# Optimization experiments

Hardware: AMD Instinct MI355X
Metric: run time of the kernel (lower is better)

The kernel has to match this reference:

```python
import jax, jax.numpy as jnp
import numpy as np

B, CN, T = 16, 22, 1000
EXP, FCH, SPD, NCLS = 300, 150, 100, 4
KS = (15, 75, 55)
_IU = np.triu_indices(SPD)
_VEC_SCALE = np.where(_IU[0] == _IU[1], 1.0, np.sqrt(2.0)).astype(np.float32)


def _ln(x, g, b, eps=1e-5):
    m = x.mean(-1, keepdims=True)
    v = x.var(-1, keepdims=True)
    return (x - m) / jnp.sqrt(v + eps) * g + b


def _block(x, w1, w2, w3, w4, g1, b1, w5, g2, b2):
    # x: (B, CN, T). Conv2d(1,1,(3,1), same) over electrode axis.
    h = jax.lax.conv_general_dilated(x[:, None], w1.reshape(1, 1, 3, 1), (1, 1),
                                     [(1, 1), (0, 0)],
                                     dimension_numbers=('NCHW', 'OIHW', 'NCHW'))[:, 0]
    # Conv2d(1, 300, (1,1)): pure channel broadcast-expand
    h = h[:, None, :, :] * w2[None, :, None, None]          # (B, EXP, CN, T)
    # Conv2dWithConstraint: depthwise spatial conv (groups=300) with max-norm=1 on each filter
    n = jnp.linalg.norm(w3, axis=1, keepdims=True)
    w3r = w3 * jnp.minimum(1.0, 1.0 / (n + 1e-12))
    h = jnp.einsum('bgct,gc->bgt', h, w3r)                  # height collapses -> (B, EXP, T)
    h = jnp.einsum('og,bgt->bot', w4, h)                    # pointwise -> (B, FCH, T)
    h = _ln(h, g1, b1)
    K = w5.shape[-1]
    # depthwise temporal conv, padding='same' (odd K)
    h = jax.lax.conv_general_dilated(h, w5, (1,), [(K // 2, K // 2)],
                                     dimension_numbers=('NCH', 'OIH', 'NCH'),
                                     feature_group_count=FCH)
    return _ln(h, g2, b2)


def setup_inputs():
    key = jax.random.key(0)
    ks = jax.random.split(key, 64)
    d = {'x': jax.random.normal(ks[0], (B, CN, T), jnp.float32)}
    i = 1
    for bi, K in zip((1, 2, 3), KS):
        d[f'b{bi}_w1'] = jax.random.normal(ks[i], (3,)) / np.sqrt(3); i += 1
        d[f'b{bi}_w2'] = jax.random.normal(ks[i], (EXP,)); i += 1
        d[f'b{bi}_w3'] = jax.random.normal(ks[i], (EXP, CN)) / np.sqrt(CN); i += 1
        d[f'b{bi}_w4'] = jax.random.normal(ks[i], (FCH, EXP)) / np.sqrt(EXP); i += 1
        d[f'b{bi}_g1'] = jnp.ones((T,)); d[f'b{bi}_b1'] = jnp.zeros((T,))
        d[f'b{bi}_w5'] = jax.random.normal(ks[i], (FCH, 1, K)) / np.sqrt(K); i += 1
        d[f'b{bi}_g2'] = jnp.ones((T,)); d[f'b{bi}_b2'] = jnp.zeros((T,))
    d['w_sconv'] = jax.random.normal(ks[i], (SPD, 3 * FCH)) / np.sqrt(3 * FCH); i += 1
    d['w_aff'] = jnp.eye(SPD) + 0.05 * jax.random.normal(ks[i], (SPD, SPD)); i += 1
    d['w_fc'] = jax.random.normal(ks[i], (NCLS, SPD * (SPD + 1) // 2)) / np.sqrt(SPD * (SPD + 1) // 2); i += 1
    d['b_fc'] = jnp.zeros((NCLS,))
    return d


def reference(x,
              b1_w1, b1_w2, b1_w3, b1_w4, b1_g1, b1_b1, b1_w5, b1_g2, b1_b2,
              b2_w1, b2_w2, b2_w3, b2_w4, b2_g1, b2_b1, b2_w5, b2_g2, b2_b2,
              b3_w1, b3_w2, b3_w3, b3_w4, b3_g1, b3_b1, b3_w5, b3_g2, b3_b2,
              w_sconv, w_aff, w_fc, b_fc):
    h1 = _block(x, b1_w1, b1_w2, b1_w3, b1_w4, b1_g1, b1_b1, b1_w5, b1_g2, b1_b2)
    h2 = _block(x, b2_w1, b2_w2, b2_w3, b2_w4, b2_g1, b2_b1, b2_w5, b2_g2, b2_b2)
    h3 = _block(x, b3_w1, b3_w2, b3_w3, b3_w4, b3_g1, b3_b1, b3_w5, b3_g2, b3_b2)
    h = jnp.concatenate([h1, h2, h3], axis=1)               # (B, 450, T)
    h = jnp.einsum('oi,bit->bot', w_sconv, h)               # (B, SPD, T)
    # PCOM: covariance pooling over time -> SPD matrix per sample
    xc = h - h.mean(-1, keepdims=True)
    cov = jnp.einsum('bit,bjt->bij', xc, xc) / (T - 1) + 1e-4 * jnp.eye(SPD)
    # AffineInvariantLayer: learnable congruence transform W P W^T
    P = jnp.einsum('ij,bjk,lk->bil', w_aff, cov, w_aff)
    # LogmLayer: matrix log via batched eigendecomposition
    w, v = jnp.linalg.eigh(P)
    L = jnp.einsum('bik,bk,bjk->bij', v, jnp.log(jnp.clip(w, 1e-6)), v)
    # Vec: upper-triangular half-vectorization (off-diag * sqrt(2)) -> 5050
    flat = L[:, _IU[0], _IU[1]] * _VEC_SCALE
    logits = flat @ w_fc.T + b_fc
    return (logits, flat)
```

## Files before the change

### kernel.cpp

```cpp
#include <hip/hip_runtime.h>

#define B_ 16
#define CN_ 22
#define T_ 1000
#define EXP_ 300
#define FCH_ 150
#define SPD_ 100
#define LDSTR 108
#define MAXSWEEP 8

static constexpr unsigned long long OFF_M2   = 0ull;
static constexpr unsigned long long OFF_HCAT = 65536ull;
static constexpr unsigned long long OFF_XC   = OFF_HCAT + 28800000ull;
static constexpr unsigned long long OFF_COV  = OFF_XC   + 6400000ull;
static constexpr unsigned long long OFF_T1   = OFF_COV  + 640000ull;
static constexpr unsigned long long OFF_P    = OFF_T1   + 640000ull;
static constexpr unsigned long long OFF_G    = OFF_XC;
static constexpr unsigned long long OFF_WC   = OFF_XC + 640000ull;

struct PrepPtrs  { const float* w1[3]; const float* w2[3]; const float* w3[3]; const float* w4[3]; };
struct FrontPtrs { const float* g1[3]; const float* b1[3]; const float* w5[3];
                   const float* g2[3]; const float* b2[3]; int K[3]; };

__device__ __forceinline__ float block_sum(float v, float* sbuf) {
  #pragma unroll
  for (int off = 32; off > 0; off >>= 1) v += __shfl_down(v, off, 64);
  const int wid  = threadIdx.x >> 6;
  const int lane = threadIdx.x & 63;
  const int nw   = blockDim.x >> 6;
  if (lane == 0) sbuf[wid] = v;
  __syncthreads();
  float r = 0.f;
  for (int w = 0; w < nw; ++w) r += sbuf[w];
  __syncthreads();
  return r;
}

__device__ __forceinline__ float dpp_shr1(float old_, float src) {
  return __builtin_bit_cast(float, __builtin_amdgcn_update_dpp(
      __builtin_bit_cast(int, old_), __builtin_bit_cast(int, src),
      0x138, 0xf, 0xf, false));
}
__device__ __forceinline__ float dpp_shl1(float old_, float src) {
  return __builtin_bit_cast(float, __builtin_amdgcn_update_dpp(
      __builtin_bit_cast(int, old_), __builtin_bit_cast(int, src),
      0x130, 0xf, 0xf, false));
}

__global__ __launch_bounds__(256) void k_prep(PrepPtrs pp, float* __restrict__ M2) {
  const int beta = blockIdx.x;
  __shared__ float w3r[EXP_*CN_];
  __shared__ float M[FCH_*CN_];
  const float* w1 = pp.w1[beta];
  const float* w2 = pp.w2[beta];
  const float* w3 = pp.w3[beta];
  const float* w4 = pp.w4[beta];

  for (int g = threadIdx.x; g < EXP_; g += 256) {
    float s = 0.f;
    for (int c = 0; c < CN_; ++c) { float w = w3[g*CN_ + c]; s += w*w; }
    float n = sqrtf(s);
    float scale = fminf(1.f, 1.f/(n + 1e-12f)) * w2[g];
    for (int c = 0; c < CN_; ++c) w3r[g*CN_ + c] = w3[g*CN_ + c] * scale;
  }
  __syncthreads();
  for (int idx = threadIdx.x; idx < FCH_*CN_; idx += 256) {
    int o = idx / CN_, c = idx - o*CN_;
    float acc = 0.f;
    for (int g = 0; g < EXP_; ++g) acc += w4[o*EXP_ + g] * w3r[g*CN_ + c];
    M[idx] = acc;
  }
  __syncthreads();
  const float k0 = w1[0], k1 = w1[1], k2 = w1[2];
  for (int idx = threadIdx.x; idx < FCH_*CN_; idx += 256) {
    int c = idx % CN_;
    float v = k1 * M[idx];
    if (c > 0)       v += k2 * M[idx - 1];
    if (c < CN_ - 1) v += k0 * M[idx + 1];
    M2[beta*FCH_*CN_ + idx] = v;
  }
}

__global__ __launch_bounds__(256) void k_front(const float* __restrict__ x,
                                               const float* __restrict__ M2,
                                               FrontPtrs fp,
                                               float* __restrict__ hcat) {
  const int wg   = blockIdx.x;
  const int beta = wg / (B_*FCH_);
  const int rem  = wg - beta*(B_*FCH_);
  const int b    = rem / FCH_;
  const int o    = rem - b*FCH_;
  const int K    = fp.K[beta];
  const int Kh   = K >> 1;

  __shared__ float m2[CN_];
  __shared__ float hb2[T_];
  __shared__ float w5s[80];
  __shared__ float red[8];

  if (threadIdx.x < CN_) m2[threadIdx.x] = M2[(beta*FCH_ + o)*CN_ + threadIdx.x];
  if (threadIdx.x < K)   w5s[threadIdx.x] = fp.w5[beta][o*K + threadIdx.x];
  __syncthreads();

  const float* xb = x + (size_t)b*CN_*T_;
  float hv[4];
  float psum = 0.f;
  #pragma unroll
  for (int e = 0; e < 4; ++e) {
    int t = threadIdx.x + 256*e;
    float acc = 0.f;
    if (t < T_) {
      #pragma unroll
      for (int c = 0; c < CN_; ++c) acc += m2[c] * xb[c*T_ + t];
    }
    hv[e] = acc; psum += acc;
  }
  float mean = block_sum(psum, red) * (1.f/T_);
  float pv = 0.f;
  #pragma unroll
  for (int e = 0; e < 4; ++e) { int t = threadIdx.x + 256*e; if (t < T_) { float d = hv[e]-mean; pv += d*d; } }
  float var = block_sum(pv, red) * (1.f/T_);
  float inv = rsqrtf(var + 1e-5f);
  const float* g1 = fp.g1[beta]; const float* b1 = fp.b1[beta];
  #pragma unroll
  for (int e = 0; e < 4; ++e) { int t = threadIdx.x + 256*e; if (t < T_) hb2[t] = (hv[e]-mean)*inv*g1[t] + b1[t]; }
  __syncthreads();

  float cv[4];
  float ps2 = 0.f;
  #pragma unroll
  for (int e = 0; e < 4; ++e) {
    int t = threadIdx.x + 256*e;
    float acc = 0.f;
    if (t < T_) {
      int lo = t - Kh;
      for (int k = 0; k < K; ++k) {
        int tt = lo + k;
        float hvv = (tt >= 0 && tt < T_) ? hb2[tt] : 0.f;
        acc += hvv * w5s[k];
      }
    }
    cv[e] = acc; ps2 += acc;
  }
  float mean2 = block_sum(ps2, red) * (1.f/T_);
  float pv2 = 0.f;
  #pragma unroll
  for (int e = 0; e < 4; ++e) { int t = threadIdx.x + 256*e; if (t < T_) { float d = cv[e]-mean2; pv2 += d*d; } }
  float var2 = block_sum(pv2, red) * (1.f/T_);
  float inv2 = rsqrtf(var2 + 1e-5f);
  const float* g2 = fp.g2[beta]; const float* b2 = fp.b2[beta];
  float* hrow = hcat + ((size_t)b*(3*FCH_) + beta*FCH_ + o)*T_;
  #pragma unroll
  for (int e = 0; e < 4; ++e) { int t = threadIdx.x + 256*e; if (t < T_) hrow[t] = (cv[e]-mean2)*inv2*g2[t] + b2[t]; }
}

__global__ __launch_bounds__(256) void k_sconv(const float* __restrict__ hcat,
                                               const float* __restrict__ wsc,
                                               float* __restrict__ xc) {
  const int b  = blockIdx.x / 10;
  const int s0 = (blockIdx.x % 10) * 10;
  __shared__ float ws[10*450];
  __shared__ float red[8];
  for (int idx = threadIdx.x; idx < 4500; idx += 256) {
    int s = idx / 450, i = idx - s*450;
    ws[idx] = wsc[(s0+s)*450 + i];
  }
  __syncthreads();
  float acc[10][4];
  #pragma unroll
  for (int s = 0; s < 10; ++s)
    #pragma unroll
    for (int e = 0; e < 4; ++e) acc[s][e] = 0.f;
  const float* hb = hcat + (size_t)b*450*T_;
  for (int i = 0; i < 450; ++i) {
    float xv[4];
    #pragma unroll
    for (int e = 0; e < 4; ++e) { int t = threadIdx.x + 256*e; xv[e] = (t < T_) ? hb[(size_t)i*T_ + t] : 0.f; }
    #pragma unroll
    for (int s = 0; s < 10; ++s) {
      float w = ws[s*450 + i];
      #pragma unroll
      for (int e = 0; e < 4; ++e) acc[s][e] += w * xv[e];
    }
  }
  for (int s = 0; s < 10; ++s) {
    float mu = block_sum(acc[s][0]+acc[s][1]+acc[s][2]+acc[s][3], red) * (1.f/T_);
    float* xr = xc + ((size_t)b*SPD_ + s0 + s)*T_;
    #pragma unroll
    for (int e = 0; e < 4; ++e) { int t = threadIdx.x + 256*e; if (t < T_) xr[t] = acc[s][e] - mu; }
  }
}

__global__ __launch_bounds__(256) void k_cov(const float* __restrict__ xc, float* __restrict__ cov) {
  const int b  = blockIdx.x / 5;
  const int j0 = (blockIdx.x % 5) * 20;
  __shared__ __align__(16) float xst[SPD_*100];
  const int it = threadIdx.x / 10;
  const int jj = threadIdx.x - it*10;
  const bool act = threadIdx.x < 250;
  double a64[4][2] = {{0.0,0.0},{0.0,0.0},{0.0,0.0},{0.0,0.0}};
  for (int ch = 0; ch < 10; ++ch) {
    __syncthreads();
    const int tc0 = ch*100;
    for (int idx = threadIdx.x; idx < SPD_*100; idx += 256) {
      int row = idx / 100, tt = idx - row*100;
      xst[idx] = xc[((size_t)b*SPD_ + row)*T_ + tc0 + tt];
    }
    __syncthreads();
    if (act) {
      float a32[4][2] = {{0,0},{0,0},{0,0},{0,0}};
      for (int t4 = 0; t4 < 100; t4 += 4) {
        float4 xi[4], xj[2];
        #pragma unroll
        for (int r = 0; r < 4; ++r) xi[r] = *(const float4*)&xst[(it + 25*r)*100 + t4];
        #pragma unroll
        for (int s = 0; s < 2; ++s) xj[s] = *(const float4*)&xst[(j0 + jj + 10*s)*100 + t4];
        #pragma unroll
        for (int r = 0; r < 4; ++r)
          #pragma unroll
          for (int s = 0; s < 2; ++s)
            a32[r][s] += xi[r].x*xj[s].x + xi[r].y*xj[s].y + xi[r].z*xj[s].z + xi[r].w*xj[s].w;
      }
      #pragma unroll
      for (int r = 0; r < 4; ++r)
        #pragma unroll
        for (int s = 0; s < 2; ++s) a64[r][s] += (double)a32[r][s];
    }
  }
  if (act) {
    #pragma unroll
    for (int r = 0; r < 4; ++r) {
      #pragma unroll
      for (int s = 0; s < 2; ++s) {
        int i = it + 25*r, j = j0 + jj + 10*s;
        double v = a64[r][s] * (1.0/999.0);
        if (i == j) v += 1e-4;
        cov[(size_t)b*SPD_*SPD_ + i*SPD_ + j] = (float)v;
      }
    }
  }
}

__global__ __launch_bounds__(256) void k_aff1(const float* __restrict__ cov,
                                              const float* __restrict__ waff,
                                              float* __restrict__ T1) {
  const int b  = blockIdx.x / 5;
  const int j0 = (blockIdx.x % 5) * 20;
  __shared__ float Cs[SPD_*101];
  __shared__ float Ws[20*100];
  for (int idx = threadIdx.x; idx < SPD_*SPD_; idx += 256) {
    int r = idx / 100, c = idx - r*100;
    Cs[r*101 + c] = cov[(size_t)b*SPD_*SPD_ + idx];
  }
  for (int idx = threadIdx.x; idx < 2000; idx += 256) {
    int jl = idx / 100, k = idx - jl*100;
    Ws[idx] = waff[(j0+jl)*100 + k];
  }
  __syncthreads();
  if (threadIdx.x < 250) {
    const int it = threadIdx.x / 10, jj = threadIdx.x % 10;
    double acc[4][2] = {{0.0,0.0},{0.0,0.0},{0.0,0.0},{0.0,0.0}};
    for (int k = 0; k < 100; ++k) {
      double cvv[4], wv[2];
      #pragma unroll
      for (int r = 0; r < 4; ++r) cvv[r] = (double)Cs[(it + 25*r)*101 + k];
      #pragma unroll
      for (int s = 0; s < 2; ++s) wv[s] = (double)Ws[(jj + 10*s)*100 + k];
      #pragma unroll
      for (int r = 0; r < 4; ++r)
        #pragma unroll
        for (int s = 0; s < 2; ++s) acc[r][s] += cvv[r]*wv[s];
    }
    #pragma unroll
    for (int r = 0; r < 4; ++r)
      #pragma unroll
      for (int s = 0; s < 2; ++s)
        T1[(size_t)b*SPD_*SPD_ + (it + 25*r)*100 + (j0 + jj + 10*s)] = (float)acc[r][s];
  }
}

__global__ __launch_bounds__(256) void k_aff2(const float* __restrict__ T1,
                                              const float* __restrict__ waff,
                                              float* __restrict__ P) {
  const int b  = blockIdx.x / 5;
  const int j0 = (blockIdx.x % 5) * 20;
  __shared__ float T1s[100*20];
  for (int idx = threadIdx.x; idx < 2000; idx += 256) {
    int k = idx / 20, jl = idx - k*20;
    T1s[idx] = T1[(size_t)b*SPD_*SPD_ + k*100 + j0 + jl];
  }
  __syncthreads();
  if (threadIdx.x < 250) {
    const int it = threadIdx.x / 10, jj = threadIdx.x % 10;
    double acc[4][2] = {{0.0,0.0},{0.0,0.0},{0.0,0.0},{0.0,0.0}};
    for (int k = 0; k < 100; ++k) {
      double wv[4], tv[2];
      #pragma unroll
      for (int r = 0; r < 4; ++r) wv[r] = (double)waff[(it + 25*r)*100 + k];
      #pragma unroll
      for (int s = 0; s < 2; ++s) tv[s] = (double)T1s[k*20 + jj + 10*s];
      #pragma unroll
      for (int r = 0; r < 4; ++r)
        #pragma unroll
        for (int s = 0; s < 2; ++s) acc[r][s] += wv[r]*tv[s];
    }
    #pragma unroll
    for (int r = 0; r < 4; ++r)
      #pragma unroll
      for (int s = 0; s < 2; ++s)
        P[(size_t)b*SPD_*SPD_ + (it + 25*r)*100 + (j0 + jj + 10*s)] = (float)acc[r][s];
  }
}

__global__ __launch_bounds__(256, 1) void k_eig(const float* __restrict__ P,
                                                float* __restrict__ Gout,
                                                double* __restrict__ WCout) {
  __shared__ __align__(16) float G[SPD_*LDSTR];
  __shared__ __align__(16) float gbuf[2][64*4];
  __shared__ __align__(16) float nbuf[64*8];
  __shared__ int fbuf[4];
  const int tid = threadIdx.x;
  const int b   = blockIdx.x;
  const int w   = tid >> 6;
  const int j   = tid & 63;
  const bool act = (j < 50);
  const int rb  = 25 * w;

  float A[25], B[25];
  const float* Pb = P + (size_t)b*SPD_*SPD_;
  #pragma unroll
  for (int i = 0; i < 25; ++i) {
    A[i] = act ? Pb[(rb+i)*SPD_ + j]      : 0.f;
    B[i] = act ? Pb[(rb+i)*SPD_ + (99-j)] : 0.f;
  }
  float pA = 0.f, pB = 0.f;
  #pragma unroll
  for (int i = 0; i < 25; ++i) { pA += A[i]*A[i]; pB += B[i]*B[i]; }
  nbuf[j*8 + w*2 + 0] = pA;
  nbuf[j*8 + w*2 + 1] = pB;
  __syncthreads();
  float nA, nB;
  {
    float4 u0 = *(const float4*)&nbuf[j*8];
    float4 u1 = *(const float4*)&nbuf[j*8+4];
    nA = (u0.x + u0.z) + (u1.x + u1.z);
    nB = (u0.y + u0.w) + (u1.y + u1.w);
  }
  float pg = 0.f;
  #pragma unroll
  for (int i = 0; i < 25; ++i) pg += A[i]*B[i];

  int par = 0;
  for (int sweep = 0; sweep < MAXSWEEP; ++sweep) {
    int swflag = 0;
    for (int r = 0; r < 99; ++r) {
      gbuf[par][j*4 + w] = pg;
      __syncthreads();
      float4 gp = *(const float4*)&gbuf[par][j*4];
      float gamma = (gp.x + gp.y) + (gp.z + gp.w);

      float cr = 1.f, sr = 0.f;
      float g2 = gamma*gamma;
      float ab = nA*nB;
      if (act && g2 > 1e-12f*ab) {
        if (g2 > 1e-6f*ab) swflag = 1;
        float tau = (nB - nA) / (2.f*gamma);
        float t = ((tau >= 0.f) ? 1.f : -1.f) / (fabsf(tau) + sqrtf(1.f + tau*tau));
        cr = rsqrtf(1.f + t*t);
        sr = t*cr;
        nA = nA - t*gamma;
        nB = nB + t*gamma;
      }
      {
        float sendN = (j == 0) ? nB : nA;
        float rNA = dpp_shr1(nA, sendN);
        float rNB = dpp_shl1(nB, nB);
        float newB = (j == 49) ? nA : rNB;
        nA = rNA; nB = newB;
      }
      pg = 0.f;
      #pragma unroll
      for (int i = 0; i < 25; ++i) {
        float na = cr*A[i] - sr*B[i];
        float nb = sr*A[i] + cr*B[i];
        float sendA = (j == 0) ? nb : na;
        float rA = dpp_shr1(na, sendA);
        float rB = dpp_shl1(nb, nb);
        A[i] = rA;
        B[i] = (j == 49) ? na : rB;
        pg += A[i]*B[i];
      }
      par ^= 1;
    }
    unsigned long long any = __ballot(swflag);
    if (j == 0) fbuf[w] = (any != 0ull) ? 1 : 0;
    __syncthreads();
    int f = fbuf[0] | fbuf[1] | fbuf[2] | fbuf[3];
    __syncthreads();
    if (!f) break;
  }

  if (act) {
    #pragma unroll
    for (int i = 0; i < 25; ++i) {
      G[j*LDSTR + rb + i]        = A[i];
      G[(50 + j)*LDSTR + rb + i] = B[i];
    }
  }
  __syncthreads();

  if (tid < SPD_) {
    const float* col = &G[tid*LDSTR];
    double s = 0.0;
    for (int i = 0; i < SPD_; ++i) { double v = (double)col[i]; s += v*v; }
    double lam = sqrt(s);
    double lc  = (lam < 1e-6) ? 1e-6 : lam;
    WCout[b*SPD_ + tid] = log(lc) / ((s > 1e-300) ? s : 1e-300);
  }
  for (int idx = tid; idx < SPD_*SPD_; idx += 256) {
    int c = idx / SPD_, i = idx - c*SPD_;
    Gout[(size_t)b*SPD_*SPD_ + idx] = G[c*LDSTR + i];
  }
}

__global__ __launch_bounds__(256) void k_lout(const float* __restrict__ Gin,
                                              const double* __restrict__ WCin,
                                              float* __restrict__ out) {
  __shared__ __align__(16) float G[SPD_*SPD_];
  __shared__ float wcs[SPD_];
  const int tid = threadIdx.x;
  const int b   = blockIdx.x;
  for (int idx = tid; idx < SPD_*SPD_; idx += 256)
    G[idx] = Gin[(size_t)b*SPD_*SPD_ + idx];
  if (tid < SPD_) wcs[tid] = (float)WCin[b*SPD_ + tid];
  __syncthreads();

  for (int tile = tid; tile < 625; tile += 256) {
    const int ti = (tile / 25) * 4;
    const int tj = (tile % 25) * 4;
    float acc[4][4];
    #pragma unroll
    for (int r = 0; r < 4; ++r)
      #pragma unroll
      for (int s = 0; s < 4; ++s) acc[r][s] = 0.f;
    for (int c = 0; c < SPD_; ++c) {
      const float* col = &G[c*SPD_];
      float4 ga = *(const float4*)&col[ti];
      float4 gb = *(const float4*)&col[tj];
      float wcv = wcs[c];
      float wa[4] = { wcv*ga.x, wcv*ga.y, wcv*ga.z, wcv*ga.w };
      float bv[4] = { gb.x, gb.y, gb.z, gb.w };
      #pragma unroll
      for (int r = 0; r < 4; ++r)
        #pragma unroll
        for (int s = 0; s < 4; ++s) acc[r][s] += wa[r]*bv[s];
    }
    const float RT2 = 1.41421356237309505f;
    #pragma unroll
    for (int r = 0; r < 4; ++r) {
      #pragma unroll
      for (int s = 0; s < 4; ++s) {
        int i = ti + r, jx = tj + s;
        if (i <= jx) {
          int idx = i*SPD_ - (i*(i+1))/2 + jx;
          out[64 + b*5050 + idx] = acc[r][s] * (i == jx ? 1.f : RT2);
        }
      }
    }
  }
}

__global__ __launch_bounds__(256) void k_fc(const float* __restrict__ wfc,
                                            const float* __restrict__ bfc,
                                            float* __restrict__ out) {
  __shared__ float red[8];
  const int b = blockIdx.x;
  const float* flat = out + 64 + b*5050;
  float a0 = 0.f, a1 = 0.f, a2 = 0.f, a3 = 0.f;
  for (int k = threadIdx.x; k < 5050; k += 256) {
    float f = flat[k];
    a0 += f * wfc[k];
    a1 += f * wfc[5050 + k];
    a2 += f * wfc[10100 + k];
    a3 += f * wfc[15150 + k];
  }
  a0 = block_sum(a0, red);
  a1 = block_sum(a1, red);
  a2 = block_sum(a2, red);
  a3 = block_sum(a3, red);
  if (threadIdx.x == 0) {
    out[b*4 + 0] = a0 + bfc[0];
    out[b*4 + 1] = a1 + bfc[1];
    out[b*4 + 2] = a2 + bfc[2];
    out[b*4 + 3] = a3 + bfc[3];
  }
}

extern "C" void kernel_launch(void* const* d_in, const int* in_sizes, int n_in,
                              void* d_out, int out_size, void* d_ws, size_t ws_size,
                              hipStream_t stream) {
  (void)in_sizes; (void)n_in; (void)out_size; (void)ws_size;
  const float* x = (const float*)d_in[0];
  const float* bw[3][9];
  for (int i = 0; i < 3; ++i)
    for (int jx = 0; jx < 9; ++jx)
      bw[i][jx] = (const float*)d_in[1 + i*9 + jx];
  const float* w_sconv = (const float*)d_in[28];
  const float* w_aff   = (const float*)d_in[29];
  const float* w_fc    = (const float*)d_in[30];
  const float* b_fc    = (const float*)d_in[31];

  char* ws = (char*)d_ws;
  float*  M2   = (float*)(ws + OFF_M2);
  float*  hcat = (float*)(ws + OFF_HCAT);
  float*  xc   = (float*)(ws + OFF_XC);
  float*  cov  = (float*)(ws + OFF_COV);
  float*  T1   = (float*)(ws + OFF_T1);
  float*  P    = (float*)(ws + OFF_P);
  float*  G    = (float*)(ws + OFF_G);
  double* WC   = (double*)(ws + OFF_WC);
  float*  out  = (float*)d_out;

  PrepPtrs pp; FrontPtrs fp;
  for (int i = 0; i < 3; ++i) {
    pp.w1[i] = bw[i][0]; pp.w2[i] = bw[i][1]; pp.w3[i] = bw[i][2]; pp.w4[i] = bw[i][3];
    fp.g1[i] = bw[i][4]; fp.b1[i] = bw[i][5]; fp.w5[i] = bw[i][6];
    fp.g2[i] = bw[i][7]; fp.b2[i] = bw[i][8];
  }
  fp.K[0] = 15; fp.K[1] = 75; fp.K[2] = 55;

  hipLaunchKernelGGL(k_prep,  dim3(3),            dim3(256), 0, stream, pp, M2);
  hipLaunchKernelGGL(k_front, dim3(3*B_*FCH_),    dim3(256), 0, stream, x, M2, fp, hcat);
  hipLaunchKernelGGL(k_sconv, dim3(B_*10),        dim3(256), 0, stream, hcat, w_sconv, xc);
  hipLaunchKernelGGL(k_cov,   dim3(B_*5),         dim3(256), 0, stream, xc, cov);
  hipLaunchKernelGGL(k_aff1,  dim3(B_*5),         dim3(256), 0, stream, cov, w_aff, T1);
  hipLaunchKernelGGL(k_aff2,  dim3(B_*5),         dim3(256), 0, stream, T1, w_aff, P);
  hipLaunchKernelGGL(k_eig,   dim3(B_),           dim3(256), 0, stream, P, G, WC);
  hipLaunchKernelGGL(k_lout,  dim3(B_),           dim3(256), 0, stream, G, WC, out);
  hipLaunchKernelGGL(k_fc,    dim3(B_),           dim3(256), 0, stream, w_fc, b_fc, out);
}
```

Measured before the change: 1.297 ms.

## Pack two matrices per Jacobi eigen block, drop convergence check, move eigenlog to output kernel

The Jacobi eigensolver now handles two batch matrices per 512-thread block, each using its own 256-thread half and shared buffers. It always runs a fixed number of sweeps instead of stopping early on a convergence vote, and the rotation is computed without branches. It writes the eigenvector columns straight to global memory, and the eigenvalue log weights are now computed in the following output kernel. This removes the per-sweep ballot and barrier, the shared staging copy and the double-precision buffer, but it halves the number of eigen blocks, makes every block barrier span more waves, and may run more sweeps than needed.

```diff
diff --git a/kernel.cpp b/kernel.cpp
--- a/kernel.cpp
+++ b/kernel.cpp
@@ -6,8 +6,7 @@
 #define EXP_ 300
 #define FCH_ 150
 #define SPD_ 100
-#define LDSTR 108
-#define MAXSWEEP 8
+#define NSWEEP 8
 
 static constexpr unsigned long long OFF_M2   = 0ull;
 static constexpr unsigned long long OFF_HCAT = 65536ull;
@@ -16,7 +15,6 @@
 static constexpr unsigned long long OFF_T1   = OFF_COV  + 640000ull;
 static constexpr unsigned long long OFF_P    = OFF_T1   + 640000ull;
 static constexpr unsigned long long OFF_G    = OFF_XC;
-static constexpr unsigned long long OFF_WC   = OFF_XC + 640000ull;
 
 struct PrepPtrs  { const float* w1[3]; const float* w2[3]; const float* w3[3]; const float* w4[3]; };
 struct FrontPtrs { const float* g1[3]; const float* b1[3]; const float* w5[3];
@@ -312,19 +310,17 @@
   }
 }
 
-__global__ __launch_bounds__(256, 1) void k_eig(const float* __restrict__ P,
-                                                float* __restrict__ Gout,
-                                                double* __restrict__ WCout) {
-  __shared__ __align__(16) float G[SPD_*LDSTR];
-  __shared__ __align__(16) float gbuf[2][64*4];
-  __shared__ __align__(16) float nbuf[64*8];
-  __shared__ int fbuf[4];
-  const int tid = threadIdx.x;
-  const int b   = blockIdx.x;
-  const int w   = tid >> 6;
-  const int j   = tid & 63;
-  const bool act = (j < 50);
-  const int rb  = 25 * w;
+__global__ __launch_bounds__(512, 1) void k_eig(const float* __restrict__ P,
+                                                float* __restrict__ Gout) {
+  __shared__ __align__(16) float gbuf[2][2][256];
+  __shared__ __align__(16) float nbuf[2][512];
+  const int tid   = threadIdx.x;
+  const int mh    = tid >> 8;
+  const int ww    = (tid >> 6) & 3;
+  const int j     = tid & 63;
+  const bool act  = (j < 50);
+  const int rb    = 25 * ww;
+  const int b     = blockIdx.x * 2 + mh;
 
   float A[25], B[25];
   const float* Pb = P + (size_t)b*SPD_*SPD_;
@@ -336,13 +332,13 @@
   float pA = 0.f, pB = 0.f;
   #pragma unroll
   for (int i = 0; i < 25; ++i) { pA += A[i]*A[i]; pB += B[i]*B[i]; }
-  nbuf[j*8 + w*2 + 0] = pA;
-  nbuf[j*8 + w*2 + 1] = pB;
+  nbuf[mh][j*8 + ww*2 + 0] = pA;
+  nbuf[mh][j*8 + ww*2 + 1] = pB;
   __syncthreads();
   float nA, nB;
   {
-    float4 u0 = *(const float4*)&nbuf[j*8];
-    float4 u1 = *(const float4*)&nbuf[j*8+4];
+    float4 u0 = *(const float4*)&nbuf[mh][j*8];
+    float4 u1 = *(const float4*)&nbuf[mh][j*8+4];
     nA = (u0.x + u0.z) + (u1.x + u1.z);
     nB = (u0.y + u0.w) + (u1.y + u1.w);
   }
@@ -351,26 +347,22 @@
   for (int i = 0; i < 25; ++i) pg += A[i]*B[i];
 
   int par = 0;
-  for (int sweep = 0; sweep < MAXSWEEP; ++sweep) {
-    int swflag = 0;
+  for (int sweep = 0; sweep < NSWEEP; ++sweep) {
     for (int r = 0; r < 99; ++r) {
-      gbuf[par][j*4 + w] = pg;
+      gbuf[mh][par][j*4 + ww] = pg;
       __syncthreads();
-      float4 gp = *(const float4*)&gbuf[par][j*4];
+      float4 gp = *(const float4*)&gbuf[mh][par][j*4];
       float gamma = (gp.x + gp.y) + (gp.z + gp.w);
 
-      float cr = 1.f, sr = 0.f;
       float g2 = gamma*gamma;
       float ab = nA*nB;
-      if (act && g2 > 1e-12f*ab) {
-        if (g2 > 1e-6f*ab) swflag = 1;
-        float tau = (nB - nA) / (2.f*gamma);
-        float t = ((tau >= 0.f) ? 1.f : -1.f) / (fabsf(tau) + sqrtf(1.f + tau*tau));
-        cr = rsqrtf(1.f + t*t);
-        sr = t*cr;
-        nA = nA - t*gamma;
-        nB = nB + t*gamma;
-      }
+      float tau = (g2 > 1e-12f*ab) ? ((nB - nA) / (2.f*gamma)) : 1e30f;
+      float t  = ((tau >= 0.f) ? 1.f : -1.f) / (fabsf(tau) + sqrtf(1.f + tau*tau));
+      float cr = rsqrtf(1.f + t*t);
+      float sr = t*cr;
+      nA = nA - t*gamma;
+      nB = nB + t*gamma;
+
       {
         float sendN = (j == 0) ? nB : nA;
         float rNA = dpp_shr1(nA, sendN);
@@ -392,39 +384,18 @@
       }
       par ^= 1;
     }
-    unsigned long long any = __ballot(swflag);
-    if (j == 0) fbuf[w] = (any != 0ull) ? 1 : 0;
-    __syncthreads();
-    int f = fbuf[0] | fbuf[1] | fbuf[2] | fbuf[3];
-    __syncthreads();
-    if (!f) break;
   }
 
   if (act) {
-    #pragma unroll
-    for (int i = 0; i < 25; ++i) {
-      G[j*LDSTR + rb + i]        = A[i];
-      G[(50 + j)*LDSTR + rb + i] = B[i];
-    }
-  }
-  __syncthreads();
-
-  if (tid < SPD_) {
-    const float* col = &G[tid*LDSTR];
-    double s = 0.0;
-    for (int i = 0; i < SPD_; ++i) { double v = (double)col[i]; s += v*v; }
-    double lam = sqrt(s);
-    double lc  = (lam < 1e-6) ? 1e-6 : lam;
-    WCout[b*SPD_ + tid] = log(lc) / ((s > 1e-300) ? s : 1e-300);
-  }
-  for (int idx = tid; idx < SPD_*SPD_; idx += 256) {
-    int c = idx / SPD_, i = idx - c*SPD_;
-    Gout[(size_t)b*SPD_*SPD_ + idx] = G[c*LDSTR + i];
+    float* Gb = Gout + (size_t)b*SPD_*SPD_;
+    #pragma unroll
+    for (int i = 0; i < 25; ++i) Gb[j*SPD_ + rb + i]        = A[i];
+    #pragma unroll
+    for (int i = 0; i < 25; ++i) Gb[(50 + j)*SPD_ + rb + i] = B[i];
   }
 }
 
 __global__ __launch_bounds__(256) void k_lout(const float* __restrict__ Gin,
-                                              const double* __restrict__ WCin,
                                               float* __restrict__ out) {
   __shared__ __align__(16) float G[SPD_*SPD_];
   __shared__ float wcs[SPD_];
@@ -432,7 +403,15 @@
   const int b   = blockIdx.x;
   for (int idx = tid; idx < SPD_*SPD_; idx += 256)
     G[idx] = Gin[(size_t)b*SPD_*SPD_ + idx];
-  if (tid < SPD_) wcs[tid] = (float)WCin[b*SPD_ + tid];
+  __syncthreads();
+  if (tid < SPD_) {
+    const float* col = &G[tid*SPD_];
+    double s = 0.0;
+    for (int i = 0; i < SPD_; ++i) { double v = (double)col[i]; s += v*v; }
+    double lam = sqrt(s);
+    double lc  = (lam < 1e-6) ? 1e-6 : lam;
+    wcs[tid] = (float)(log(lc) / ((s > 1e-300) ? s : 1e-300));
+  }
   __syncthreads();
 
   for (int tile = tid; tile < 625; tile += 256) {
@@ -518,7 +497,6 @@
   float*  T1   = (float*)(ws + OFF_T1);
   float*  P    = (float*)(ws + OFF_P);
   float*  G    = (float*)(ws + OFF_G);
-  double* WC   = (double*)(ws + OFF_WC);
   float*  out  = (float*)d_out;
 
   PrepPtrs pp; FrontPtrs fp;
@@ -535,7 +513,7 @@
   hipLaunchKernelGGL(k_cov,   dim3(B_*5),         dim3(256), 0, stream, xc, cov);
   hipLaunchKernelGGL(k_aff1,  dim3(B_*5),         dim3(256), 0, stream, cov, w_aff, T1);
   hipLaunchKernelGGL(k_aff2,  dim3(B_*5),         dim3(256), 0, stream, T1, w_aff, P);
-  hipLaunchKernelGGL(k_eig,   dim3(B_),           dim3(256), 0, stream, P, G, WC);
-  hipLaunchKernelGGL(k_lout,  dim3(B_),           dim3(256), 0, stream, G, WC, out);
+  hipLaunchKernelGGL(k_eig,   dim3(B_/2),         dim3(512), 0, stream, P, G);
+  hipLaunchKernelGGL(k_lout,  dim3(B_),           dim3(256), 0, stream, G, out);
   hipLaunchKernelGGL(k_fc,    dim3(B_),           dim3(256), 0, stream, w_fc, b_fc, out);
 }
```

Result: slower. 1.610 ms (+24.1%).
